# Performance work log

Hardware: AMD Instinct MI355X
Metric: run time of the kernel (lower is better)

## Reference

```python
import jax, jax.numpy as jnp
import numpy as np

N, E, H, C = 50000, 800000, 4, 32   # nodes, edges, heads, per-head channels
EMB = 64                              # embedding_dim
VOCAB = 1000                          # input_dim (label vocab)


def _gat_layer(x, src, dst, W, a_src, a_dst, b):
    """PyG GATConv (concat heads, negative_slope=0.2, self-loops already in src/dst)."""
    n = x.shape[0]
    h = (x @ W).reshape(n, H, -1)                 # [N,H,C]
    al_s = (h * a_src).sum(-1)                    # [N,H]
    al_d = (h * a_dst).sum(-1)                    # [N,H]
    e = jax.nn.leaky_relu(al_s[src] + al_d[dst], 0.2)   # [E',H]
    m = jax.ops.segment_max(e, dst, num_segments=n)     # segment softmax (stable)
    p = jnp.exp(e - m[dst])
    s = jax.ops.segment_sum(p, dst, num_segments=n)
    alpha = p / (s[dst] + 1e-16)                  # [E',H]
    out = jax.ops.segment_sum(h[src] * alpha[..., None], dst, num_segments=n)
    return out.reshape(n, -1) + b                 # [N,H*C]


def setup_inputs() -> dict:
    key = jax.random.key(0)
    ks = jax.random.split(key, 16)
    def w(k, shape):
        return jax.random.normal(k, shape, jnp.float32) * 0.1
    return dict(
        label=jax.random.randint(ks[0], (N,), 0, VOCAB),
        edge_index=jax.random.randint(ks[1], (2, E), 0, N),
        weight=jax.random.uniform(ks[2], (E,), jnp.float32),
        request_quantity=jax.random.uniform(ks[3], (N,), jnp.float32),
        emb_table=w(ks[4], (VOCAB, EMB)),
        req_W=w(ks[5], (1, EMB)),
        req_b=jnp.zeros((EMB,), jnp.float32),
        W0=w(ks[6], (2 * EMB, H * C)), a_src0=w(ks[7], (H, C)), a_dst0=w(ks[8], (H, C)), b0=jnp.zeros((H * C,), jnp.float32),
        W1=w(ks[9], (H * C, H * C)), a_src1=w(ks[10], (H, C)), a_dst1=w(ks[11], (H, C)), b1=jnp.zeros((H * C,), jnp.float32),
        W2=w(ks[12], (H * C, H * C)), a_src2=w(ks[13], (H, C)), a_dst2=w(ks[14], (H, C)), b2=jnp.zeros((H * C,), jnp.float32),
    )


def reference(label, edge_index, weight, request_quantity, emb_table, req_W, req_b,
              W0, a_src0, a_dst0, b0, W1, a_src1, a_dst1, b1, W2, a_src2, a_dst2, b2):
    del weight  # GATConv(edge_dim=None): edge weights are not used in attention
    x_emb = emb_table[label]                                  # [N,EMB]
    rq = request_quantity
    rq = (rq - rq.mean()) / (rq.std(ddof=1) + 1e-6)           # torch std uses ddof=1
    req = rq[:, None] @ req_W + req_b                         # [N,EMB]
    x = jnp.concatenate([x_emb, req], axis=-1)                # [N,2*EMB]
    # PyG GATConv adds self-loops by default
    loops = jnp.arange(N)
    src = jnp.concatenate([edge_index[0], loops])
    dst = jnp.concatenate([edge_index[1], loops])
    gelu = lambda t: jax.nn.gelu(t, approximate=False)        # torch nn.GELU is exact
    x = gelu(_gat_layer(x, src, dst, W0, a_src0, a_dst0, b0))
    x = gelu(_gat_layer(x, src, dst, W1, a_src1, a_dst1, b1))
    x = gelu(_gat_layer(x, src, dst, W2, a_src2, a_dst2, b2))
    return x
```

## Files before the change

kernel.cpp:

```cpp
#include <hip/hip_runtime.h>
#include <hip/hip_fp16.h>
#include <math.h>

#define NN 50000
#define NE 800000
#define HC 128
#define EMB 64
#define STATS_BLOCKS 64
#define NB 196
#define HIST_BLOCKS 196
#define WPREP_BLOCKS 192
#define WT_ROW 136
#define GEMM_BLOCKS 782

typedef _Float16 f16x8 __attribute__((ext_vector_type(8)));
typedef float f32x4 __attribute__((ext_vector_type(4)));

__device__ __forceinline__ float lrelu(float x) { return x > 0.0f ? x : 0.2f * x; }
__device__ __forceinline__ float gelu_f(float x) {
    return 0.5f * x * (1.0f + erff(x * 0.70710678118654752440f));
}
__device__ __forceinline__ float sel4(float4 v, int h) {
    float r = v.x;
    r = (h == 1) ? v.y : r;
    r = (h == 2) ? v.z : r;
    r = (h == 3) ? v.w : r;
    return r;
}
__device__ __forceinline__ f16x8 cvt8(float4 a, float4 b) {
    f16x8 v;
    v[0] = (_Float16)a.x; v[1] = (_Float16)a.y; v[2] = (_Float16)a.z; v[3] = (_Float16)a.w;
    v[4] = (_Float16)b.x; v[5] = (_Float16)b.y; v[6] = (_Float16)b.z; v[7] = (_Float16)b.w;
    return v;
}

__global__ void prep_kernel(const float* __restrict__ rq, float* __restrict__ stats,
                            const int* __restrict__ dst, int* __restrict__ bucketCnt,
                            const float* __restrict__ W0, const float* __restrict__ W1,
                            const float* __restrict__ W2, _Float16* __restrict__ wt) {
    __shared__ float ls[4], ls2[4];
    __shared__ int cnt[NB];
    if (blockIdx.x < STATS_BLOCKS) {
        int i = blockIdx.x * 256 + threadIdx.x;
        float s = 0.f, s2 = 0.f;
        for (; i < NN; i += STATS_BLOCKS * 256) {
            float v = rq[i];
            s += v; s2 += v * v;
        }
        #pragma unroll
        for (int off = 32; off > 0; off >>= 1) {
            s  += __shfl_down(s, off);
            s2 += __shfl_down(s2, off);
        }
        int lane = threadIdx.x & 63, wid = threadIdx.x >> 6;
        if (lane == 0) { ls[wid] = s; ls2[wid] = s2; }
        __syncthreads();
        if (threadIdx.x == 0) {
            atomicAdd(&stats[0], ls[0] + ls[1] + ls[2] + ls[3]);
            atomicAdd(&stats[1], ls2[0] + ls2[1] + ls2[2] + ls2[3]);
        }
    } else if (blockIdx.x < STATS_BLOCKS + HIST_BLOCKS) {
        int bb = blockIdx.x - STATS_BLOCKS;
        for (int i = threadIdx.x; i < NB; i += 256) cnt[i] = 0;
        __syncthreads();
        int base = bb * 4096;
        #pragma unroll
        for (int it = 0; it < 16; it++) {
            int i = base + it * 256 + threadIdx.x;
            if (i < NE) atomicAdd(&cnt[dst[i] >> 8], 1);
        }
        __syncthreads();
        for (int i = threadIdx.x; i < NB; i += 256)
            if (cnt[i]) atomicAdd(&bucketCnt[i], cnt[i]);
    } else {
        int bb = blockIdx.x - STATS_BLOCKS - HIST_BLOCKS;
        int l = bb >> 6, blk = bb & 63;
        const float* W = (l == 0) ? W0 : (l == 1) ? W1 : W2;
        int idx = blk * 256 + threadIdx.x;
        int n = idx >> 7, k = idx & 127;
        wt[(size_t)l * 128 * WT_ROW + n * WT_ROW + k] = (_Float16)W[k * 128 + n];
    }
}

__device__ __forceinline__ void scan_buckets(const int* __restrict__ bucketCnt,
                                             int* sIncl ) {
    int t = threadIdx.x;
    int v = (t < NB) ? bucketCnt[t] : 0;
    sIncl[t] = v;
    __syncthreads();
    #pragma unroll
    for (int off = 1; off < 256; off <<= 1) {
        int add = (t >= off) ? sIncl[t - off] : 0;
        __syncthreads();
        sIncl[t] += add;
        __syncthreads();
    }
}

__device__ __forceinline__ void mfma_epilogue(_Float16* sWt, _Float16* sX,
        const float* __restrict__ a_src, const float* __restrict__ a_dst,
        __half* __restrict__ h, float* __restrict__ als, float* __restrict__ ald,
        int row0) {
    int t = threadIdx.x;
    int w = t >> 6, l = t & 63;
    int col = l & 15, quad = l >> 4;

    f16x8 afr[4];
    #pragma unroll
    for (int ks = 0; ks < 4; ks++)
        afr[ks] = *(const f16x8*)&sX[(w * 16 + col) * WT_ROW + ks * 32 + quad * 8];

    f32x4 zero = {0.f, 0.f, 0.f, 0.f};
    f32x4 acc[8];
    #pragma unroll
    for (int nt = 0; nt < 8; nt++) acc[nt] = zero;
    #pragma unroll
    for (int nt = 0; nt < 8; nt++) {
        #pragma unroll
        for (int ks = 0; ks < 4; ks++) {
            f16x8 bfr = *(const f16x8*)&sWt[(nt * 16 + col) * WT_ROW + ks * 32 + quad * 8];
            acc[nt] = __builtin_amdgcn_mfma_f32_16x16x32_f16(afr[ks], bfr, acc[nt], 0, 0, 0);
        }
    }
    __syncthreads();

    _Float16* sOut = sWt;
    #pragma unroll
    for (int nt = 0; nt < 8; nt++)
        #pragma unroll
        for (int r = 0; r < 4; r++)
            sOut[(w * 16 + quad * 4 + r) * WT_ROW + nt * 16 + col] = (_Float16)acc[nt][r];
    __builtin_amdgcn_wave_barrier();
    #pragma unroll
    for (int i = 0; i < 4; i++) {
        int u = l + 64 * i;
        int r = u >> 4, off = (u & 15) * 8;
        int rr = row0 + w * 16 + r;
        f16x8 v = *(const f16x8*)&sOut[(w * 16 + r) * WT_ROW + off];
        if (rr < NN) *(f16x8*)(h + (size_t)rr * 128 + off) = v;
    }

    float as[8], ad[8];
    #pragma unroll
    for (int nt = 0; nt < 8; nt++) {
        as[nt] = a_src[nt * 16 + col];
        ad[nt] = a_dst[nt * 16 + col];
    }
    #pragma unroll
    for (int r = 0; r < 4; r++) {
        float ps[4], pd[4];
        #pragma unroll
        for (int hd = 0; hd < 4; hd++) {
            ps[hd] = acc[2 * hd][r] * as[2 * hd] + acc[2 * hd + 1][r] * as[2 * hd + 1];
            pd[hd] = acc[2 * hd][r] * ad[2 * hd] + acc[2 * hd + 1][r] * ad[2 * hd + 1];
            ps[hd] += __shfl_xor(ps[hd], 1); pd[hd] += __shfl_xor(pd[hd], 1);
            ps[hd] += __shfl_xor(ps[hd], 2); pd[hd] += __shfl_xor(pd[hd], 2);
            ps[hd] += __shfl_xor(ps[hd], 4); pd[hd] += __shfl_xor(pd[hd], 4);
            ps[hd] += __shfl_xor(ps[hd], 8); pd[hd] += __shfl_xor(pd[hd], 8);
        }
        int rr = row0 + w * 16 + quad * 4 + r;
        if (col == 0 && rr < NN) {
            *(float4*)(als + (size_t)rr * 4) = make_float4(ps[0], ps[1], ps[2], ps[3]);
            *(float4*)(ald + (size_t)rr * 4) = make_float4(pd[0], pd[1], pd[2], pd[3]);
        }
    }
}

__launch_bounds__(256)
__global__ void gemm0_binA_kernel(const _Float16* __restrict__ wt,
                                  const float* __restrict__ a_src, const float* __restrict__ a_dst,
                                  __half* __restrict__ h, float* __restrict__ als,
                                  float* __restrict__ ald,
                                  const int* __restrict__ label, const float* __restrict__ rq,
                                  const float* __restrict__ emb, const float* __restrict__ reqW,
                                  const float* __restrict__ reqb, const float* __restrict__ stats,
                                  const int* __restrict__ src, const int* __restrict__ dst,
                                  const int* __restrict__ bucketCnt, int* __restrict__ gcur,
                                  int2* __restrict__ edge_tmp) {
    extern __shared__ char smem[];
    if (blockIdx.x >= GEMM_BLOCKS) {
        int bb = blockIdx.x - GEMM_BLOCKS;
        int* sIncl  = (int*)smem;
        int* sBaseE = sIncl + 256;
        int* cnt    = sBaseE + 256;
        int* cur    = cnt + NB;
        int t = threadIdx.x;
        scan_buckets(bucketCnt, sIncl);
        {
            int v = (t < NB) ? bucketCnt[t] : 0;
            sBaseE[t] = sIncl[t] - v;
        }
        for (int i = t; i < NB; i += 256) cnt[i] = 0;
        __syncthreads();
        int base = bb * 4096;
        int d[16], s[16];
        #pragma unroll
        for (int it = 0; it < 16; it++) {
            int i = base + it * 256 + t;
            bool ok = i < NE;
            d[it] = ok ? dst[i] : -1;
            s[it] = ok ? src[i] : 0;
            if (ok) atomicAdd(&cnt[d[it] >> 8], 1);
        }
        __syncthreads();
        for (int i = t; i < NB; i += 256)
            cur[i] = cnt[i] ? (sBaseE[i] + atomicAdd(&gcur[i], cnt[i])) : 0;
        __syncthreads();
        #pragma unroll
        for (int it = 0; it < 16; it++) {
            if (d[it] >= 0) {
                int b = d[it] >> 8;
                int pos = atomicAdd(&cur[b], 1);
                edge_tmp[pos] = make_int2(s[it], d[it] & 255);
            }
        }
        return;
    }
    _Float16* sWt = (_Float16*)smem;
    _Float16* sX  = sWt + 128 * WT_ROW;
    int t = threadIdx.x;
    int row0 = blockIdx.x * 64;

    {
        const f16x8* g = (const f16x8*)wt;
        f16x8* s = (f16x8*)sWt;
        #pragma unroll
        for (int i = 0; i < 9; i++) {
            int idx = t + 256 * i;
            if (idx < 128 * WT_ROW / 8) s[idx] = g[idx];
        }
    }
    {
        float sum = stats[0], sumsq = stats[1];
        float mean = sum / (float)NN;
        float var = (sumsq - sum * sum / (float)NN) / (float)(NN - 1);
        float inv = 1.0f / (sqrtf(var) + 1e-6f);
        #pragma unroll
        for (int i = 0; i < 4; i++) {
            int idx = t + 256 * i;
            int r = idx >> 4;
            int q = idx & 15;
            int rr = row0 + r;
            f16x8 v;
            #pragma unroll
            for (int j = 0; j < 8; j++) v[j] = (_Float16)0.f;
            if (rr < NN) {
                if (q < 8) {
                    const float4* er = (const float4*)(emb + (size_t)label[rr] * EMB);
                    v = cvt8(er[q * 2], er[q * 2 + 1]);
                } else {
                    int j4 = (q - 8) * 2;
                    float4 w0 = ((const float4*)reqW)[j4],     b0 = ((const float4*)reqb)[j4];
                    float4 w1 = ((const float4*)reqW)[j4 + 1], b1 = ((const float4*)reqb)[j4 + 1];
                    float r2 = (rq[rr] - mean) * inv;
                    v = cvt8(make_float4(r2 * w0.x + b0.x, r2 * w0.y + b0.y,
                                         r2 * w0.z + b0.z, r2 * w0.w + b0.w),
                             make_float4(r2 * w1.x + b1.x, r2 * w1.y + b1.y,
                                         r2 * w1.z + b1.z, r2 * w1.w + b1.w));
                }
            }
            *(f16x8*)&sX[r * WT_ROW + q * 8] = v;
        }
    }
    __syncthreads();
    mfma_epilogue(sWt, sX, a_src, a_dst, h, als, ald, row0);
}

__global__ void binB_kernel(const int2* __restrict__ edge_tmp, const int* __restrict__ bucketCnt,
                            int* __restrict__ row_start, int* __restrict__ src_sorted) {
    __shared__ int sIncl[256];
    __shared__ int ldeg[256];
    __shared__ int lexcl[256];
    __shared__ int lcur[256];
    __shared__ int s_base, s_end;
    int b = blockIdx.x, t = threadIdx.x;
    scan_buckets(bucketCnt, sIncl);
    if (t == 0) {
        s_end = sIncl[b];
        s_base = sIncl[b] - bucketCnt[b];
    }
    ldeg[t] = 0;
    __syncthreads();
    int base = s_base, endb = s_end;
    for (int i = base + t; i < endb; i += 256)
        atomicAdd(&ldeg[edge_tmp[i].y], 1);
    __syncthreads();
    int v = ldeg[t];
    lexcl[t] = v;
    __syncthreads();
    #pragma unroll
    for (int off = 1; off < 256; off <<= 1) {
        int add = (t >= off) ? lexcl[t - off] : 0;
        __syncthreads();
        lexcl[t] += add;
        __syncthreads();
    }
    int excl = lexcl[t] - v;
    int node = b * 256 + t;
    if (node <= NN) row_start[node] = base + excl;
    lcur[t] = excl;
    __syncthreads();
    for (int i = base + t; i < endb; i += 256) {
        int2 e = edge_tmp[i];
        int pos = atomicAdd(&lcur[e.y], 1);
        src_sorted[base + pos] = e.x;
    }
}

__launch_bounds__(256)
__global__ void gemm_ln_kernel(const __half* __restrict__ xh, const _Float16* __restrict__ wt,
                               const float* __restrict__ a_src, const float* __restrict__ a_dst,
                               __half* __restrict__ h, float* __restrict__ als,
                               float* __restrict__ ald) {
    extern __shared__ char smem[];
    _Float16* sWt = (_Float16*)smem;
    int t = threadIdx.x;
    int w = t >> 6, l = t & 63;
    int col = l & 15, quad = l >> 4;
    int row0 = blockIdx.x * 64;

    {
        const f16x8* g = (const f16x8*)wt;
        f16x8* s = (f16x8*)sWt;
        #pragma unroll
        for (int i = 0; i < 9; i++) {
            int idx = t + 256 * i;
            if (idx < 128 * WT_ROW / 8) s[idx] = g[idx];
        }
    }
    __syncthreads();

    f16x8 afr[4];
    {
        int rr = row0 + w * 16 + col;
        const __half* xp = xh + (size_t)rr * 128;
        #pragma unroll
        for (int ks = 0; ks < 4; ks++)
            afr[ks] = *(const f16x8*)(xp + ks * 32 + quad * 8);
    }

    f32x4 zero = {0.f, 0.f, 0.f, 0.f};
    f32x4 acc[8];
    #pragma unroll
    for (int nt = 0; nt < 8; nt++) acc[nt] = zero;
    #pragma unroll
    for (int nt = 0; nt < 8; nt++) {
        #pragma unroll
        for (int ks = 0; ks < 4; ks++) {
            f16x8 bfr = *(const f16x8*)&sWt[(nt * 16 + col) * WT_ROW + ks * 32 + quad * 8];
            acc[nt] = __builtin_amdgcn_mfma_f32_16x16x32_f16(afr[ks], bfr, acc[nt], 0, 0, 0);
        }
    }
    __syncthreads();

    _Float16* sOut = sWt;
    #pragma unroll
    for (int nt = 0; nt < 8; nt++)
        #pragma unroll
        for (int r = 0; r < 4; r++)
            sOut[(w * 16 + quad * 4 + r) * WT_ROW + nt * 16 + col] = (_Float16)acc[nt][r];
    __builtin_amdgcn_wave_barrier();
    #pragma unroll
    for (int i = 0; i < 4; i++) {
        int u = l + 64 * i;
        int r = u >> 4, off = (u & 15) * 8;
        int rr = row0 + w * 16 + r;
        f16x8 v = *(const f16x8*)&sOut[(w * 16 + r) * WT_ROW + off];
        if (rr < NN) *(f16x8*)(h + (size_t)rr * 128 + off) = v;
    }

    float as[8], ad[8];
    #pragma unroll
    for (int nt = 0; nt < 8; nt++) {
        as[nt] = a_src[nt * 16 + col];
        ad[nt] = a_dst[nt * 16 + col];
    }
    #pragma unroll
    for (int r = 0; r < 4; r++) {
        float ps[4], pd[4];
        #pragma unroll
        for (int hd = 0; hd < 4; hd++) {
            ps[hd] = acc[2 * hd][r] * as[2 * hd] + acc[2 * hd + 1][r] * as[2 * hd + 1];
            pd[hd] = acc[2 * hd][r] * ad[2 * hd] + acc[2 * hd + 1][r] * ad[2 * hd + 1];
            ps[hd] += __shfl_xor(ps[hd], 1); pd[hd] += __shfl_xor(pd[hd], 1);
            ps[hd] += __shfl_xor(ps[hd], 2); pd[hd] += __shfl_xor(pd[hd], 2);
            ps[hd] += __shfl_xor(ps[hd], 4); pd[hd] += __shfl_xor(pd[hd], 4);
            ps[hd] += __shfl_xor(ps[hd], 8); pd[hd] += __shfl_xor(pd[hd], 8);
        }
        int rr = row0 + w * 16 + quad * 4 + r;
        if (col == 0 && rr < NN) {
            *(float4*)(als + (size_t)rr * 4) = make_float4(ps[0], ps[1], ps[2], ps[3]);
            *(float4*)(ald + (size_t)rr * 4) = make_float4(pd[0], pd[1], pd[2], pd[3]);
        }
    }
}

template <int FINAL>
__launch_bounds__(256)
__global__ void agg_kernel(const __half* __restrict__ h, const float* __restrict__ als_,
                           const float* __restrict__ ald_, const int* __restrict__ row_start,
                           const int* __restrict__ src_sorted, const float* __restrict__ bias,
                           float* __restrict__ outf, __half* __restrict__ outh) {
    __shared__ int2 lds_sp[4][4][130];
    int wid  = threadIdx.x >> 6;
    int lane = threadIdx.x & 63;
    int g    = lane >> 4;
    int cg   = lane & 15;
    int c0   = cg * 8;
    int head = cg >> 2;

    int nb = blockIdx.x * 16 + wid * 4;
    if (nb >= NN) return;
    int node = nb + g;

    int rs = row_start[node];
    int re = row_start[node + 1];
    int start = __shfl(rs, 0);
    int end   = __shfl(re, 48);
    int b1 = __shfl(rs, 16), b2 = __shfl(rs, 32), b3 = __shfl(rs, 48);

    float4 adv = *(const float4*)(ald_ + (size_t)node * 4);
    float4 avs = *(const float4*)(als_ + (size_t)node * 4);

    float p_self = __expf(lrelu(sel4(avs, head) + sel4(adv, head)));
    float s_sum = p_self;
    float acc[8];
    {
        f16x8 hv = *(const f16x8*)(h + (size_t)node * 128 + c0);
        #pragma unroll
        for (int j = 0; j < 8; j++) acc[j] = (float)hv[j] * p_self;
    }

    for (int base = start; base < end; base += 128) {
        int j0 = base + lane, j1 = base + 64 + lane;
        bool v0 = j0 < end, v1 = j1 < end;
        int my0 = v0 ? src_sorted[j0] : 0;
        int my1 = v1 ? src_sorted[j1] : 0;
        float4 av0 = *(const float4*)(als_ + (size_t)my0 * 4);
        float4 av1 = *(const float4*)(als_ + (size_t)my1 * 4);
        int o0 = (j0 >= b1) + (j0 >= b2) + (j0 >= b3);
        int o1 = (j1 >= b1) + (j1 >= b2) + (j1 >= b3);
        float4 d0 = *(const float4*)(ald_ + (size_t)(nb + (o0 > 3 ? 3 : o0)) * 4);
        float4 d1 = *(const float4*)(ald_ + (size_t)(nb + (o1 > 3 ? 3 : o1)) * 4);
        lds_sp[wid][0][lane] = make_int2(my0, __float_as_int(__expf(lrelu(av0.x + d0.x))));
        lds_sp[wid][1][lane] = make_int2(my0, __float_as_int(__expf(lrelu(av0.y + d0.y))));
        lds_sp[wid][2][lane] = make_int2(my0, __float_as_int(__expf(lrelu(av0.z + d0.z))));
        lds_sp[wid][3][lane] = make_int2(my0, __float_as_int(__expf(lrelu(av0.w + d0.w))));
        lds_sp[wid][0][64 + lane] = make_int2(my1, __float_as_int(__expf(lrelu(av1.x + d1.x))));
        lds_sp[wid][1][64 + lane] = make_int2(my1, __float_as_int(__expf(lrelu(av1.y + d1.y))));
        lds_sp[wid][2][64 + lane] = make_int2(my1, __float_as_int(__expf(lrelu(av1.z + d1.z))));
        lds_sp[wid][3][64 + lane] = make_int2(my1, __float_as_int(__expf(lrelu(av1.w + d1.w))));
        __builtin_amdgcn_wave_barrier();

        int lo  = rs > base ? rs : base;
        int hiw = base + 128;
        int hi  = re < hiw ? re : hiw;
        for (int k = lo; k < hi; k += 16) {
            float p[16];
            const __half* ap[16];
            #pragma unroll
            for (int i = 0; i < 16; i++) {
                int e = k + i;
                bool val = e < hi;
                int ec = (val ? e : hi - 1) - base;
                int2 sp = lds_sp[wid][head][ec];
                p[i] = val ? __int_as_float(sp.y) : 0.f;
                ap[i] = h + (size_t)sp.x * 128 + c0;
            }
            f16x8 raw[16];
            #pragma unroll
            for (int i = 0; i < 16; i++)
                raw[i] = *(const f16x8*)ap[i];
            #pragma unroll
            for (int i = 0; i < 16; i++) {
                s_sum += p[i];
                #pragma unroll
                for (int jj = 0; jj < 8; jj++)
                    acc[jj] += (float)raw[i][jj] * p[i];
            }
        }
        __builtin_amdgcn_wave_barrier();
    }

    float invs = 1.0f / (s_sum + 1e-16f);
    float4 bv0 = *(const float4*)(bias + c0);
    float4 bv1 = *(const float4*)(bias + c0 + 4);
    float ob[8] = {bv0.x, bv0.y, bv0.z, bv0.w, bv1.x, bv1.y, bv1.z, bv1.w};
    float o8[8];
    #pragma unroll
    for (int jj = 0; jj < 8; jj++) o8[jj] = gelu_f(acc[jj] * invs + ob[jj]);
    if (FINAL) {
        float* op = outf + (size_t)node * 128 + c0;
        *(float4*)op       = make_float4(o8[0], o8[1], o8[2], o8[3]);
        *(float4*)(op + 4) = make_float4(o8[4], o8[5], o8[6], o8[7]);
    } else {
        f16x8 hv;
        #pragma unroll
        for (int jj = 0; jj < 8; jj++) hv[jj] = (_Float16)o8[jj];
        *(f16x8*)(outh + (size_t)node * 128 + c0) = hv;
    }
}

extern "C" void kernel_launch(void* const* d_in, const int* in_sizes, int n_in,
                              void* d_out, int out_size, void* d_ws, size_t ws_size,
                              hipStream_t stream) {
    const int*   label = (const int*)d_in[0];
    const int*   eidx  = (const int*)d_in[1];
    const float* rq    = (const float*)d_in[3];
    const float* emb   = (const float*)d_in[4];
    const float* reqW  = (const float*)d_in[5];
    const float* reqb  = (const float*)d_in[6];
    const float* W[3]    = {(const float*)d_in[7],  (const float*)d_in[11], (const float*)d_in[15]};
    const float* asrc[3] = {(const float*)d_in[8],  (const float*)d_in[12], (const float*)d_in[16]};
    const float* adst[3] = {(const float*)d_in[9],  (const float*)d_in[13], (const float*)d_in[17]};
    const float* bias[3] = {(const float*)d_in[10], (const float*)d_in[14], (const float*)d_in[18]};

    const int* e_src = eidx;
    const int* e_dst = eidx + NE;

    char* ws = (char*)d_ws;
    size_t off = 0;
    auto A = [&](size_t n) { size_t o = off; off += (n + 255) & ~(size_t)255; return o; };
    size_t o_bcnt  = A(256 * 4);
    size_t o_gcur  = A(256 * 4);
    size_t o_stats = A(8);
    size_t zero_bytes = off;
    size_t o_row   = A((size_t)(NN + 1) * 4);
    size_t o_etmp  = A((size_t)NE * 8);
    size_t o_srcS  = A((size_t)NE * 4);
    size_t o_wt    = A((size_t)3 * 128 * WT_ROW * 2);
    size_t o_x     = A((size_t)NN * 128 * 2);
    size_t o_h     = A((size_t)NN * 128 * 2);
    size_t o_als   = A((size_t)NN * 4 * 4);
    size_t o_ald   = A((size_t)NN * 4 * 4);
    (void)ws_size; (void)n_in; (void)in_sizes; (void)out_size;

    int*      bcnt  = (int*)(ws + o_bcnt);
    int*      gcur  = (int*)(ws + o_gcur);
    float*    stats = (float*)(ws + o_stats);
    int*      rowst = (int*)(ws + o_row);
    int2*     etmp  = (int2*)(ws + o_etmp);
    int*      srcS  = (int*)(ws + o_srcS);
    _Float16* wt    = (_Float16*)(ws + o_wt);
    __half*   xh    = (__half*)(ws + o_x);
    __half*   h     = (__half*)(ws + o_h);
    float*    als   = (float*)(ws + o_als);
    float*    ald   = (float*)(ws + o_ald);

    (void)hipMemsetAsync(ws, 0, zero_bytes, stream);

    const int smem_l0 = (128 + 64) * WT_ROW * 2;
    const int smem_ln = 128 * WT_ROW * 2;
    const int agg_blocks = (NN + 15) / 16;

    prep_kernel<<<STATS_BLOCKS + HIST_BLOCKS + WPREP_BLOCKS, 256, 0, stream>>>(
        rq, stats, e_dst, bcnt, W[0], W[1], W[2], wt);
    gemm0_binA_kernel<<<GEMM_BLOCKS + HIST_BLOCKS, 256, smem_l0, stream>>>(
        wt, asrc[0], adst[0], h, als, ald, label, rq, emb, reqW, reqb, stats,
        e_src, e_dst, bcnt, gcur, etmp);
    binB_kernel<<<NB, 256, 0, stream>>>(etmp, bcnt, rowst, srcS);
    agg_kernel<0><<<agg_blocks, 256, 0, stream>>>(h, als, ald, rowst, srcS, bias[0],
                                                  nullptr, xh);
    gemm_ln_kernel<<<GEMM_BLOCKS, 256, smem_ln, stream>>>(
        xh, wt + (size_t)1 * 128 * WT_ROW, asrc[1], adst[1], h, als, ald);
    agg_kernel<0><<<agg_blocks, 256, 0, stream>>>(h, als, ald, rowst, srcS, bias[1],
                                                  nullptr, xh);
    gemm_ln_kernel<<<GEMM_BLOCKS, 256, smem_ln, stream>>>(
        xh, wt + (size_t)2 * 128 * WT_ROW, asrc[2], adst[2], h, als, ald);
    agg_kernel<1><<<agg_blocks, 256, 0, stream>>>(h, als, ald, rowst, srcS, bias[2],
                                                  (float*)d_out, nullptr);
}
```

Before: 285.6 us.

## Fuse aggregation with next layer's GEMM into one kernel per layer

Merges the edge aggregation (softmax-weighted gather plus GELU) of layer i with the projection GEMM and attention-logit computation of layer i+1. Each block aggregates 64 nodes into shared memory, then runs MFMA on them directly, so the intermediate activation never round-trips through global memory and two launches are removed. Ping-pong h/als/ald buffers avoid read-write races between blocks. The weight tile is no longer staged in LDS but read from global memory per wave, and each block now does four serial aggregation rounds, which lowers parallelism and occupancy in the gather phase.

Measured after the change: 291.0 us. About the same (+1.9%).

```diff
diff --git a/kernel.cpp b/kernel.cpp
--- a/kernel.cpp
+++ b/kernel.cpp
@@ -308,65 +308,143 @@
 }
 
 __launch_bounds__(256)
-__global__ void gemm_ln_kernel(const __half* __restrict__ xh, const _Float16* __restrict__ wt,
-                               const float* __restrict__ a_src, const float* __restrict__ a_dst,
-                               __half* __restrict__ h, float* __restrict__ als,
-                               float* __restrict__ ald) {
-    extern __shared__ char smem[];
-    _Float16* sWt = (_Float16*)smem;
+__global__ void layer_fused_kernel(const __half* __restrict__ hp, const float* __restrict__ alsp,
+                                   const float* __restrict__ aldp, const int* __restrict__ row_start,
+                                   const int* __restrict__ src_sorted, const float* __restrict__ biasp,
+                                   const _Float16* __restrict__ wt,
+                                   const float* __restrict__ a_src, const float* __restrict__ a_dst,
+                                   __half* __restrict__ ho, float* __restrict__ also_,
+                                   float* __restrict__ aldo) {
+    __shared__ _Float16 sX[64 * WT_ROW];
+    __shared__ int2 lds_sp[4][4][130];
     int t = threadIdx.x;
-    int w = t >> 6, l = t & 63;
-    int col = l & 15, quad = l >> 4;
+    int w = t >> 6, lane = t & 63;
+    int g    = lane >> 4;
+    int cg   = lane & 15;
+    int c0   = cg * 8;
+    int head = cg >> 2;
     int row0 = blockIdx.x * 64;
 
-    {
-        const f16x8* g = (const f16x8*)wt;
-        f16x8* s = (f16x8*)sWt;
-        #pragma unroll
-        for (int i = 0; i < 9; i++) {
-            int idx = t + 256 * i;
-            if (idx < 128 * WT_ROW / 8) s[idx] = g[idx];
-        }
-    }
-    __syncthreads();
-
+    for (int round = 0; round < 4; round++) {
+        int nb = row0 + w * 16 + round * 4;
+        if (nb >= NN) continue;
+        int node = nb + g;
+
+        int rs = row_start[node];
+        int re = row_start[node + 1];
+        int start = __shfl(rs, 0);
+        int end   = __shfl(re, 48);
+        int b1 = __shfl(rs, 16), b2 = __shfl(rs, 32), b3 = __shfl(rs, 48);
+
+        float4 adv = *(const float4*)(aldp + (size_t)node * 4);
+        float4 avs = *(const float4*)(alsp + (size_t)node * 4);
+
+        float p_self = __expf(lrelu(sel4(avs, head) + sel4(adv, head)));
+        float s_sum = p_self;
+        float acc[8];
+        {
+            f16x8 hv = *(const f16x8*)(hp + (size_t)node * 128 + c0);
+            #pragma unroll
+            for (int j = 0; j < 8; j++) acc[j] = (float)hv[j] * p_self;
+        }
+
+        for (int base = start; base < end; base += 128) {
+            int j0 = base + lane, j1 = base + 64 + lane;
+            bool v0 = j0 < end, v1 = j1 < end;
+            int my0 = v0 ? src_sorted[j0] : 0;
+            int my1 = v1 ? src_sorted[j1] : 0;
+            float4 av0 = *(const float4*)(alsp + (size_t)my0 * 4);
+            float4 av1 = *(const float4*)(alsp + (size_t)my1 * 4);
+            int o0 = (j0 >= b1) + (j0 >= b2) + (j0 >= b3);
+            int o1 = (j1 >= b1) + (j1 >= b2) + (j1 >= b3);
+            float4 d0 = *(const float4*)(aldp + (size_t)(nb + (o0 > 3 ? 3 : o0)) * 4);
+            float4 d1 = *(const float4*)(aldp + (size_t)(nb + (o1 > 3 ? 3 : o1)) * 4);
+            lds_sp[w][0][lane] = make_int2(my0, __float_as_int(__expf(lrelu(av0.x + d0.x))));
+            lds_sp[w][1][lane] = make_int2(my0, __float_as_int(__expf(lrelu(av0.y + d0.y))));
+            lds_sp[w][2][lane] = make_int2(my0, __float_as_int(__expf(lrelu(av0.z + d0.z))));
+            lds_sp[w][3][lane] = make_int2(my0, __float_as_int(__expf(lrelu(av0.w + d0.w))));
+            lds_sp[w][0][64 + lane] = make_int2(my1, __float_as_int(__expf(lrelu(av1.x + d1.x))));
+            lds_sp[w][1][64 + lane] = make_int2(my1, __float_as_int(__expf(lrelu(av1.y + d1.y))));
+            lds_sp[w][2][64 + lane] = make_int2(my1, __float_as_int(__expf(lrelu(av1.z + d1.z))));
+            lds_sp[w][3][64 + lane] = make_int2(my1, __float_as_int(__expf(lrelu(av1.w + d1.w))));
+            __builtin_amdgcn_wave_barrier();
+
+            int lo  = rs > base ? rs : base;
+            int hiw = base + 128;
+            int hi  = re < hiw ? re : hiw;
+            for (int k = lo; k < hi; k += 8) {
+                float p[8];
+                const __half* ap[8];
+                #pragma unroll
+                for (int i = 0; i < 8; i++) {
+                    int e = k + i;
+                    bool val = e < hi;
+                    int ec = (val ? e : hi - 1) - base;
+                    int2 sp = lds_sp[w][head][ec];
+                    p[i] = val ? __int_as_float(sp.y) : 0.f;
+                    ap[i] = hp + (size_t)sp.x * 128 + c0;
+                }
+                f16x8 raw[8];
+                #pragma unroll
+                for (int i = 0; i < 8; i++)
+                    raw[i] = *(const f16x8*)ap[i];
+                #pragma unroll
+                for (int i = 0; i < 8; i++) {
+                    s_sum += p[i];
+                    #pragma unroll
+                    for (int jj = 0; jj < 8; jj++)
+                        acc[jj] += (float)raw[i][jj] * p[i];
+                }
+            }
+            __builtin_amdgcn_wave_barrier();
+        }
+
+        float invs = 1.0f / (s_sum + 1e-16f);
+        float4 bv0 = *(const float4*)(biasp + c0);
+        float4 bv1 = *(const float4*)(biasp + c0 + 4);
+        float ob[8] = {bv0.x, bv0.y, bv0.z, bv0.w, bv1.x, bv1.y, bv1.z, bv1.w};
+        f16x8 o;
+        #pragma unroll
+        for (int jj = 0; jj < 8; jj++)
+            o[jj] = (_Float16)gelu_f(acc[jj] * invs + ob[jj]);
+        *(f16x8*)&sX[(w * 16 + round * 4 + g) * WT_ROW + c0] = o;
+    }
+    __builtin_amdgcn_wave_barrier();
+
+    int col = cg, quad = g;
     f16x8 afr[4];
-    {
-        int rr = row0 + w * 16 + col;
-        const __half* xp = xh + (size_t)rr * 128;
-        #pragma unroll
-        for (int ks = 0; ks < 4; ks++)
-            afr[ks] = *(const f16x8*)(xp + ks * 32 + quad * 8);
-    }
+    #pragma unroll
+    for (int ks = 0; ks < 4; ks++)
+        afr[ks] = *(const f16x8*)&sX[(w * 16 + col) * WT_ROW + ks * 32 + quad * 8];
+    __builtin_amdgcn_wave_barrier();
 
     f32x4 zero = {0.f, 0.f, 0.f, 0.f};
-    f32x4 acc[8];
-    #pragma unroll
-    for (int nt = 0; nt < 8; nt++) acc[nt] = zero;
+    f32x4 acc2[8];
+    #pragma unroll
+    for (int nt = 0; nt < 8; nt++) acc2[nt] = zero;
     #pragma unroll
     for (int nt = 0; nt < 8; nt++) {
         #pragma unroll
         for (int ks = 0; ks < 4; ks++) {
-            f16x8 bfr = *(const f16x8*)&sWt[(nt * 16 + col) * WT_ROW + ks * 32 + quad * 8];
-            acc[nt] = __builtin_amdgcn_mfma_f32_16x16x32_f16(afr[ks], bfr, acc[nt], 0, 0, 0);
-        }
-    }
-    __syncthreads();
-
-    _Float16* sOut = sWt;
+            f16x8 bfr = *(const f16x8*)&wt[(nt * 16 + col) * WT_ROW + ks * 32 + quad * 8];
+            acc2[nt] = __builtin_amdgcn_mfma_f32_16x16x32_f16(afr[ks], bfr, acc2[nt], 0, 0, 0);
+        }
+    }
+
+    _Float16* sOut = sX;
     #pragma unroll
     for (int nt = 0; nt < 8; nt++)
         #pragma unroll
         for (int r = 0; r < 4; r++)
-            sOut[(w * 16 + quad * 4 + r) * WT_ROW + nt * 16 + col] = (_Float16)acc[nt][r];
+            sOut[(w * 16 + quad * 4 + r) * WT_ROW + nt * 16 + col] = (_Float16)acc2[nt][r];
     __builtin_amdgcn_wave_barrier();
     #pragma unroll
     for (int i = 0; i < 4; i++) {
-        int u = l + 64 * i;
-        int r = u >> 4, off = (u & 15) * 8;
+        int u = lane + 64 * i;
+        int r = u >> 4, off2 = (u & 15) * 8;
         int rr = row0 + w * 16 + r;
-        f16x8 v = *(const f16x8*)&sOut[(w * 16 + r) * WT_ROW + off];
-        if (rr < NN) *(f16x8*)(h + (size_t)rr * 128 + off) = v;
+        f16x8 v = *(const f16x8*)&sOut[(w * 16 + r) * WT_ROW + off2];
+        if (rr < NN) *(f16x8*)(ho + (size_t)rr * 128 + off2) = v;
     }
 
     float as[8], ad[8];
@@ -380,8 +458,8 @@
         float ps[4], pd[4];
         #pragma unroll
         for (int hd = 0; hd < 4; hd++) {
-            ps[hd] = acc[2 * hd][r] * as[2 * hd] + acc[2 * hd + 1][r] * as[2 * hd + 1];
-            pd[hd] = acc[2 * hd][r] * ad[2 * hd] + acc[2 * hd + 1][r] * ad[2 * hd + 1];
+            ps[hd] = acc2[2 * hd][r] * as[2 * hd] + acc2[2 * hd + 1][r] * as[2 * hd + 1];
+            pd[hd] = acc2[2 * hd][r] * ad[2 * hd] + acc2[2 * hd + 1][r] * ad[2 * hd + 1];
             ps[hd] += __shfl_xor(ps[hd], 1); pd[hd] += __shfl_xor(pd[hd], 1);
             ps[hd] += __shfl_xor(ps[hd], 2); pd[hd] += __shfl_xor(pd[hd], 2);
             ps[hd] += __shfl_xor(ps[hd], 4); pd[hd] += __shfl_xor(pd[hd], 4);
@@ -389,18 +467,17 @@
         }
         int rr = row0 + w * 16 + quad * 4 + r;
         if (col == 0 && rr < NN) {
-            *(float4*)(als + (size_t)rr * 4) = make_float4(ps[0], ps[1], ps[2], ps[3]);
-            *(float4*)(ald + (size_t)rr * 4) = make_float4(pd[0], pd[1], pd[2], pd[3]);
-        }
-    }
-}
-
-template <int FINAL>
+            *(float4*)(also_ + (size_t)rr * 4) = make_float4(ps[0], ps[1], ps[2], ps[3]);
+            *(float4*)(aldo + (size_t)rr * 4) = make_float4(pd[0], pd[1], pd[2], pd[3]);
+        }
+    }
+}
+
 __launch_bounds__(256)
-__global__ void agg_kernel(const __half* __restrict__ h, const float* __restrict__ als_,
-                           const float* __restrict__ ald_, const int* __restrict__ row_start,
-                           const int* __restrict__ src_sorted, const float* __restrict__ bias,
-                           float* __restrict__ outf, __half* __restrict__ outh) {
+__global__ void agg_final_kernel(const __half* __restrict__ h, const float* __restrict__ als_,
+                                 const float* __restrict__ ald_, const int* __restrict__ row_start,
+                                 const int* __restrict__ src_sorted, const float* __restrict__ bias,
+                                 float* __restrict__ outf) {
     __shared__ int2 lds_sp[4][4][130];
     int wid  = threadIdx.x >> 6;
     int lane = threadIdx.x & 63;
@@ -489,16 +566,9 @@
     float o8[8];
     #pragma unroll
     for (int jj = 0; jj < 8; jj++) o8[jj] = gelu_f(acc[jj] * invs + ob[jj]);
-    if (FINAL) {
-        float* op = outf + (size_t)node * 128 + c0;
-        *(float4*)op       = make_float4(o8[0], o8[1], o8[2], o8[3]);
-        *(float4*)(op + 4) = make_float4(o8[4], o8[5], o8[6], o8[7]);
-    } else {
-        f16x8 hv;
-        #pragma unroll
-        for (int jj = 0; jj < 8; jj++) hv[jj] = (_Float16)o8[jj];
-        *(f16x8*)(outh + (size_t)node * 128 + c0) = hv;
-    }
+    float* op = outf + (size_t)node * 128 + c0;
+    *(float4*)op       = make_float4(o8[0], o8[1], o8[2], o8[3]);
+    *(float4*)(op + 4) = make_float4(o8[4], o8[5], o8[6], o8[7]);
 }
 
 extern "C" void kernel_launch(void* const* d_in, const int* in_sizes, int n_in,
@@ -529,10 +599,12 @@
     size_t o_etmp  = A((size_t)NE * 8);
     size_t o_srcS  = A((size_t)NE * 4);
     size_t o_wt    = A((size_t)3 * 128 * WT_ROW * 2);
-    size_t o_x     = A((size_t)NN * 128 * 2);
-    size_t o_h     = A((size_t)NN * 128 * 2);
-    size_t o_als   = A((size_t)NN * 4 * 4);
-    size_t o_ald   = A((size_t)NN * 4 * 4);
+    size_t o_h0    = A((size_t)NN * 128 * 2);
+    size_t o_h1    = A((size_t)NN * 128 * 2);
+    size_t o_als0  = A((size_t)NN * 4 * 4);
+    size_t o_ald0  = A((size_t)NN * 4 * 4);
+    size_t o_als1  = A((size_t)NN * 4 * 4);
+    size_t o_ald1  = A((size_t)NN * 4 * 4);
     (void)ws_size; (void)n_in; (void)in_sizes; (void)out_size;
 
     int*      bcnt  = (int*)(ws + o_bcnt);
@@ -542,31 +614,29 @@
     int2*     etmp  = (int2*)(ws + o_etmp);
     int*      srcS  = (int*)(ws + o_srcS);
     _Float16* wt    = (_Float16*)(ws + o_wt);
-    __half*   xh    = (__half*)(ws + o_x);
-    __half*   h     = (__half*)(ws + o_h);
-    float*    als   = (float*)(ws + o_als);
-    float*    ald   = (float*)(ws + o_ald);
+    __half*   h0    = (__half*)(ws + o_h0);
+    __half*   h1    = (__half*)(ws + o_h1);
+    float*    als0  = (float*)(ws + o_als0);
+    float*    ald0  = (float*)(ws + o_ald0);
+    float*    als1  = (float*)(ws + o_als1);
+    float*    ald1  = (float*)(ws + o_ald1);
 
     (void)hipMemsetAsync(ws, 0, zero_bytes, stream);
 
     const int smem_l0 = (128 + 64) * WT_ROW * 2;
-    const int smem_ln = 128 * WT_ROW * 2;
-    const int agg_blocks = (NN + 15) / 16;
 
     prep_kernel<<<STATS_BLOCKS + HIST_BLOCKS + WPREP_BLOCKS, 256, 0, stream>>>(
         rq, stats, e_dst, bcnt, W[0], W[1], W[2], wt);
     gemm0_binA_kernel<<<GEMM_BLOCKS + HIST_BLOCKS, 256, smem_l0, stream>>>(
-        wt, asrc[0], adst[0], h, als, ald, label, rq, emb, reqW, reqb, stats,
+        wt, asrc[0], adst[0], h0, als0, ald0, label, rq, emb, reqW, reqb, stats,
         e_src, e_dst, bcnt, gcur, etmp);
     binB_kernel<<<NB, 256, 0, stream>>>(etmp, bcnt, rowst, srcS);
-    agg_kernel<0><<<agg_blocks, 256, 0, stream>>>(h, als, ald, rowst, srcS, bias[0],
-                                                  nullptr, xh);
-    gemm_ln_kernel<<<GEMM_BLOCKS, 256, smem_ln, stream>>>(
-        xh, wt + (size_t)1 * 128 * WT_ROW, asrc[1], adst[1], h, als, ald);
-    agg_kernel<0><<<agg_blocks, 256, 0, stream>>>(h, als, ald, rowst, srcS, bias[1],
-                                                  nullptr, xh);
-    gemm_ln_kernel<<<GEMM_BLOCKS, 256, smem_ln, stream>>>(
-        xh, wt + (size_t)2 * 128 * WT_ROW, asrc[2], adst[2], h, als, ald);
-    agg_kernel<1><<<agg_blocks, 256, 0, stream>>>(h, als, ald, rowst, srcS, bias[2],
-                                                  (float*)d_out, nullptr);
-}
+    layer_fused_kernel<<<GEMM_BLOCKS, 256, 0, stream>>>(
+        h0, als0, ald0, rowst, srcS, bias[0],
+        wt + (size_t)1 * 128 * WT_ROW, asrc[1], adst[1], h1, als1, ald1);
+    layer_fused_kernel<<<GEMM_BLOCKS, 256, 0, stream>>>(
+        h1, als1, ald1, rowst, srcS, bias[1],
+        wt + (size_t)2 * 128 * WT_ROW, asrc[2], adst[2], h0, als0, ald0);
+    agg_final_kernel<<<(NN + 15) / 16, 256, 0, stream>>>(
+        h0, als0, ald0, rowst, srcS, bias[2], (float*)d_out);
+}
```
